# Optimization experiments

Hardware: AMD Instinct MI355X
Metric: run time of the kernel (lower is better)

The kernel has to match this reference:

```python
import jax, jax.numpy as jnp
import numpy as np

N_NODES = 100000

def _glorot(key, shape):
    lim = np.sqrt(6.0 / (shape[0] + shape[1])).astype(np.float32)
    return jax.random.uniform(key, shape, jnp.float32, -lim, lim)

def setup_inputs() -> dict:
    key = jax.random.key(0)
    ks = jax.random.split(key, 9)
    x = jax.random.normal(ks[0], (N_NODES, 256), jnp.float32)
    edge_index = jax.random.randint(ks[1], (2, 1600000), 0, N_NODES, jnp.int32)
    dims = [(256, 256), (256, 256), (256, 40)]
    params = {}
    for i, (din, dout) in enumerate(dims):
        params[f"Wl{i}"] = _glorot(ks[2 + 2 * i], (din, dout))   # neighbor (lin_l) weight
        params[f"Wr{i}"] = _glorot(ks[3 + 2 * i], (din, dout))   # root (lin_r) weight
        params[f"b{i}"] = jnp.zeros((dout,), jnp.float32)
    return {"x": x, "edge_index": edge_index, **params}

def _sage_conv(x, src, dst, Wl, Wr, b):
    # mean-aggregate neighbor features at destination nodes, then linear
    msg_sum = jax.ops.segment_sum(x[src], dst, num_segments=N_NODES)      # [N, d]
    deg = jax.ops.segment_sum(jnp.ones((src.shape[0],), x.dtype), dst,
                              num_segments=N_NODES)                       # [N]
    mean = msg_sum / jnp.maximum(deg, 1.0)[:, None]
    return mean @ Wl + x @ Wr + b

def reference(x, edge_index, Wl0, Wr0, b0, Wl1, Wr1, b1, Wl2, Wr2, b2):
    src, dst = edge_index[0], edge_index[1]
    h = jax.nn.relu(_sage_conv(x, src, dst, Wl0, Wr0, b0))
    h = jax.nn.relu(_sage_conv(h, src, dst, Wl1, Wr1, b1))
    h = _sage_conv(h, src, dst, Wl2, Wr2, b2)
    return jax.nn.log_softmax(h, axis=1)
```

## Files before the change

kernel.cpp:

```cpp
#include <hip/hip_runtime.h>
#include <hip/hip_bf16.h>
#include <math.h>

#define N_NODES 100000
#define N_EDGES 1600000
#define DIN 256
#define KTOT 512
#define SLOTS 64

typedef __attribute__((ext_vector_type(8))) short frag_ab;
typedef __attribute__((ext_vector_type(4))) float frag_cd;

__device__ inline unsigned short f2bf(float f) {
    union { float f; unsigned u; } v; v.f = f;
    unsigned r = v.u + 0x7FFF + ((v.u >> 16) & 1);
    return (unsigned short)(r >> 16);
}
__device__ inline float bf2f(unsigned u16) {
    union { unsigned u; float f; } v; v.u = u16 << 16;
    return v.f;
}
__device__ inline float bf_lo(unsigned u) {
    union { unsigned u; float f; } v; v.u = u << 16; return v.f;
}
__device__ inline float bf_hi(unsigned u) {
    union { unsigned u; float f; } v; v.u = u & 0xffff0000u; return v.f;
}

__global__ void build_bucket(const int* __restrict__ src, const int* __restrict__ dst,
                             int* __restrict__ cnt, int* __restrict__ col, int nE) {
    int e = blockIdx.x * blockDim.x + threadIdx.x;
    if (e >= nE) return;
    int d = dst[e];
    int pos = atomicAdd(&cnt[d], 1);
    if (pos < SLOTS) col[(size_t)d * SLOTS + pos] = src[e];
}

__global__ void conv_f32_bf16(const float* __restrict__ x, unsigned short* __restrict__ y, int n4) {
    int i = blockIdx.x * blockDim.x + threadIdx.x;
    if (i >= n4) return;
    float4 v = ((const float4*)x)[i];
    uint2 o;
    o.x = (unsigned)f2bf(v.x) | ((unsigned)f2bf(v.y) << 16);
    o.y = (unsigned)f2bf(v.z) | ((unsigned)f2bf(v.w) << 16);
    ((uint2*)y)[i] = o;
}

__global__ void conv_weights(const float* __restrict__ Wl0, const float* __restrict__ Wr0,
                             const float* __restrict__ Wl1, const float* __restrict__ Wr1,
                             const float* __restrict__ Wl2, const float* __restrict__ Wr2,
                             unsigned short* __restrict__ Wt0, unsigned short* __restrict__ Wt1,
                             unsigned short* __restrict__ Wl2t, unsigned short* __restrict__ Wr2t) {
    int idx = blockIdx.x * blockDim.x + threadIdx.x;
    if (idx < 262144) {
        const float* Wl = (idx < 131072) ? Wl0 : Wl1;
        const float* Wr = (idx < 131072) ? Wr0 : Wr1;
        unsigned short* Wt = (idx < 131072) ? Wt0 : Wt1;
        int i = idx & 131071;
        int n = i >> 9, k = i & 511;
        float v = (k < 256) ? Wl[k * 256 + n] : Wr[(k - 256) * 256 + n];
        Wt[i] = f2bf(v);
    } else if (idx < 294912) {
        const float* W = (idx < 278528) ? Wl2 : Wr2;
        unsigned short* Wt = (idx < 278528) ? Wl2t : Wr2t;
        int i = (idx - 262144) & 16383;
        int n = i >> 8, k = i & 255;
        Wt[i] = f2bf((n < 40) ? W[k * 40 + n] : 0.f);
    }
}

__global__ __launch_bounds__(256) void gather_mean_bf(
    const int* __restrict__ cnt, const int* __restrict__ col,
    const unsigned short* __restrict__ h, unsigned short* __restrict__ mean, int nNodes) {
    int node = blockIdx.x * 4 + (threadIdx.x >> 6);
    int lane = threadIdx.x & 63;
    if (node >= nNodes) return;
    int deg = cnt[node];
    int nd = (deg < SLOTS) ? deg : SLOTS;
    const int* cp = col + (size_t)node * SLOTS;
    int half = lane >> 5;
    int l = lane & 31;
    float a0 = 0, a1 = 0, a2 = 0, a3 = 0, a4 = 0, a5 = 0, a6 = 0, a7 = 0;
    int e = 0;
    for (; e + 8 <= nd; e += 8) {
        int s0 = cp[e + half];
        int s1 = cp[e + 2 + half];
        int s2 = cp[e + 4 + half];
        int s3 = cp[e + 6 + half];
        uint4 v0 = *(const uint4*)(h + (size_t)s0 * DIN + l * 8);
        uint4 v1 = *(const uint4*)(h + (size_t)s1 * DIN + l * 8);
        uint4 v2 = *(const uint4*)(h + (size_t)s2 * DIN + l * 8);
        uint4 v3 = *(const uint4*)(h + (size_t)s3 * DIN + l * 8);
        a0 += bf_lo(v0.x); a1 += bf_hi(v0.x); a2 += bf_lo(v0.y); a3 += bf_hi(v0.y);
        a4 += bf_lo(v0.z); a5 += bf_hi(v0.z); a6 += bf_lo(v0.w); a7 += bf_hi(v0.w);
        a0 += bf_lo(v1.x); a1 += bf_hi(v1.x); a2 += bf_lo(v1.y); a3 += bf_hi(v1.y);
        a4 += bf_lo(v1.z); a5 += bf_hi(v1.z); a6 += bf_lo(v1.w); a7 += bf_hi(v1.w);
        a0 += bf_lo(v2.x); a1 += bf_hi(v2.x); a2 += bf_lo(v2.y); a3 += bf_hi(v2.y);
        a4 += bf_lo(v2.z); a5 += bf_hi(v2.z); a6 += bf_lo(v2.w); a7 += bf_hi(v2.w);
        a0 += bf_lo(v3.x); a1 += bf_hi(v3.x); a2 += bf_lo(v3.y); a3 += bf_hi(v3.y);
        a4 += bf_lo(v3.z); a5 += bf_hi(v3.z); a6 += bf_lo(v3.w); a7 += bf_hi(v3.w);
    }
    for (; e + 2 <= nd; e += 2) {
        int s = cp[e + half];
        uint4 v = *(const uint4*)(h + (size_t)s * DIN + l * 8);
        a0 += bf_lo(v.x); a1 += bf_hi(v.x); a2 += bf_lo(v.y); a3 += bf_hi(v.y);
        a4 += bf_lo(v.z); a5 += bf_hi(v.z); a6 += bf_lo(v.w); a7 += bf_hi(v.w);
    }
    if (e < nd && half == 0) {
        int s = cp[e];
        uint4 v = *(const uint4*)(h + (size_t)s * DIN + l * 8);
        a0 += bf_lo(v.x); a1 += bf_hi(v.x); a2 += bf_lo(v.y); a3 += bf_hi(v.y);
        a4 += bf_lo(v.z); a5 += bf_hi(v.z); a6 += bf_lo(v.w); a7 += bf_hi(v.w);
    }
    a0 += __shfl_xor(a0, 32); a1 += __shfl_xor(a1, 32);
    a2 += __shfl_xor(a2, 32); a3 += __shfl_xor(a3, 32);
    a4 += __shfl_xor(a4, 32); a5 += __shfl_xor(a5, 32);
    a6 += __shfl_xor(a6, 32); a7 += __shfl_xor(a7, 32);
    if (half == 0) {
        float inv = 1.0f / fmaxf((float)deg, 1.0f);
        uint4 o;
        o.x = (unsigned)f2bf(a0 * inv) | ((unsigned)f2bf(a1 * inv) << 16);
        o.y = (unsigned)f2bf(a2 * inv) | ((unsigned)f2bf(a3 * inv) << 16);
        o.z = (unsigned)f2bf(a4 * inv) | ((unsigned)f2bf(a5 * inv) << 16);
        o.w = (unsigned)f2bf(a6 * inv) | ((unsigned)f2bf(a7 * inv) << 16);
        *(uint4*)(mean + (size_t)node * DIN + l * 8) = o;
    }
}

__global__ __launch_bounds__(256) void gather_mean64(
    const int* __restrict__ cnt, const int* __restrict__ col,
    const unsigned short* __restrict__ z, unsigned short* __restrict__ mz, int nNodes) {
    int node = blockIdx.x * 4 + (threadIdx.x >> 6);
    int lane = threadIdx.x & 63;
    if (node >= nNodes) return;
    int deg = cnt[node];
    int nd = (deg < SLOTS) ? deg : SLOTS;
    const int* cp = col + (size_t)node * SLOTS;
    int g = lane >> 4;
    int l = lane & 15;
    float a0 = 0, a1 = 0, a2 = 0, a3 = 0;
    int e = 0;
    for (; e + 8 <= nd; e += 8) {
        int s0 = cp[e + g];
        int s1 = cp[e + 4 + g];
        uint2 v0 = *(const uint2*)(z + (size_t)s0 * 64 + l * 4);
        uint2 v1 = *(const uint2*)(z + (size_t)s1 * 64 + l * 4);
        a0 += bf_lo(v0.x); a1 += bf_hi(v0.x); a2 += bf_lo(v0.y); a3 += bf_hi(v0.y);
        a0 += bf_lo(v1.x); a1 += bf_hi(v1.x); a2 += bf_lo(v1.y); a3 += bf_hi(v1.y);
    }
    for (; e + 4 <= nd; e += 4) {
        int s = cp[e + g];
        uint2 v = *(const uint2*)(z + (size_t)s * 64 + l * 4);
        a0 += bf_lo(v.x); a1 += bf_hi(v.x); a2 += bf_lo(v.y); a3 += bf_hi(v.y);
    }
    int rem = nd - e;
    if (g < rem) {
        int s = cp[e + g];
        uint2 v = *(const uint2*)(z + (size_t)s * 64 + l * 4);
        a0 += bf_lo(v.x); a1 += bf_hi(v.x); a2 += bf_lo(v.y); a3 += bf_hi(v.y);
    }
    a0 += __shfl_xor(a0, 16); a1 += __shfl_xor(a1, 16);
    a2 += __shfl_xor(a2, 16); a3 += __shfl_xor(a3, 16);
    a0 += __shfl_xor(a0, 32); a1 += __shfl_xor(a1, 32);
    a2 += __shfl_xor(a2, 32); a3 += __shfl_xor(a3, 32);
    if (lane < 16) {
        float inv = 1.0f / fmaxf((float)deg, 1.0f);
        uint2 o;
        o.x = (unsigned)f2bf(a0 * inv) | ((unsigned)f2bf(a1 * inv) << 16);
        o.y = (unsigned)f2bf(a2 * inv) | ((unsigned)f2bf(a3 * inv) << 16);
        *(uint2*)(mz + (size_t)node * 64 + l * 4) = o;
    }
}

template <bool RELU>
__global__ __launch_bounds__(256) void sage_mfma(
    const unsigned short* __restrict__ mean, const unsigned short* __restrict__ h,
    const unsigned short* __restrict__ Wt, const float* __restrict__ bias,
    unsigned short* __restrict__ out, int nNodes) {
    __shared__ unsigned short sA[64][32];
    __shared__ unsigned short sB[256][32];

    int tid = threadIdx.x;
    int wave = tid >> 6;
    int lane = tid & 63;
    int lrow = lane & 15;
    int quad = lane >> 4;
    int node0 = blockIdx.x * 64;

    frag_cd acc[4][4];
#pragma unroll
    for (int mi = 0; mi < 4; mi++)
#pragma unroll
        for (int ni = 0; ni < 4; ni++) acc[mi][ni] = (frag_cd){0.f, 0.f, 0.f, 0.f};

    int ar = tid >> 2;
    int ak = (tid & 3) * 8;
    int aNode = node0 + ar;

    for (int kb = 0; kb < KTOT; kb += 32) {
        {
            const unsigned short* srcp = (kb < 256)
                ? (mean + (size_t)aNode * DIN + kb + ak)
                : (h + (size_t)aNode * DIN + (kb - 256) + ak);
            uint4 av = {0u, 0u, 0u, 0u};
            if (aNode < nNodes) av = *(const uint4*)srcp;
            *(uint4*)(&sA[ar][ak]) = av;
        }
        {
            const unsigned short* wp = Wt + (size_t)tid * KTOT + kb;
#pragma unroll
            for (int j = 0; j < 4; j++)
                *(uint4*)(&sB[tid][j * 8]) = *(const uint4*)(wp + j * 8);
        }
        __syncthreads();

        frag_ab aF[4], bF[4];
#pragma unroll
        for (int mi = 0; mi < 4; mi++)
            aF[mi] = *(const frag_ab*)(&sA[mi * 16 + lrow][quad * 8]);
#pragma unroll
        for (int ni = 0; ni < 4; ni++)
            bF[ni] = *(const frag_ab*)(&sB[(wave * 4 + ni) * 16 + lrow][quad * 8]);

#pragma unroll
        for (int mi = 0; mi < 4; mi++)
#pragma unroll
            for (int ni = 0; ni < 4; ni++)
                acc[mi][ni] = __builtin_amdgcn_mfma_f32_16x16x32_bf16(
                    aF[mi], bF[ni], acc[mi][ni], 0, 0, 0);
        __syncthreads();
    }

#pragma unroll
    for (int ni = 0; ni < 4; ni++) {
        int colc = (wave * 4 + ni) * 16 + lrow;
        float bv = bias[colc];
#pragma unroll
        for (int mi = 0; mi < 4; mi++) {
#pragma unroll
            for (int r = 0; r < 4; r++) {
                int node = node0 + mi * 16 + quad * 4 + r;
                if (node < nNodes) {
                    float v = acc[mi][ni][r] + bv;
                    if (RELU) v = fmaxf(v, 0.f);
                    out[(size_t)node * 256 + colc] = f2bf(v);
                }
            }
        }
    }
}

__global__ __launch_bounds__(256) void mfma_lin64(
    const unsigned short* __restrict__ h, const unsigned short* __restrict__ Wt,
    unsigned short* __restrict__ z, int nNodes) {
    __shared__ unsigned short sA[64][32];
    __shared__ unsigned short sB[64][32];

    int tid = threadIdx.x;
    int wave = tid >> 6;
    int lane = tid & 63;
    int lrow = lane & 15;
    int quad = lane >> 4;
    int node0 = blockIdx.x * 64;

    frag_cd acc[4];
#pragma unroll
    for (int ni = 0; ni < 4; ni++) acc[ni] = (frag_cd){0.f, 0.f, 0.f, 0.f};

    int ar = tid >> 2;
    int ak = (tid & 3) * 8;
    int aNode = node0 + ar;

    for (int kb = 0; kb < 256; kb += 32) {
        uint4 av = {0u, 0u, 0u, 0u};
        if (aNode < nNodes) av = *(const uint4*)(h + (size_t)aNode * DIN + kb + ak);
        *(uint4*)(&sA[ar][ak]) = av;
        *(uint4*)(&sB[ar][ak]) = *(const uint4*)(Wt + (size_t)ar * 256 + kb + ak);
        __syncthreads();

        frag_ab aF = *(const frag_ab*)(&sA[wave * 16 + lrow][quad * 8]);
#pragma unroll
        for (int ni = 0; ni < 4; ni++) {
            frag_ab bF = *(const frag_ab*)(&sB[ni * 16 + lrow][quad * 8]);
            acc[ni] = __builtin_amdgcn_mfma_f32_16x16x32_bf16(aF, bF, acc[ni], 0, 0, 0);
        }
        __syncthreads();
    }

#pragma unroll
    for (int ni = 0; ni < 4; ni++) {
        int colc = ni * 16 + lrow;
#pragma unroll
        for (int r = 0; r < 4; r++) {
            int node = node0 + wave * 16 + quad * 4 + r;
            if (node < nNodes)
                z[(size_t)node * 64 + colc] = f2bf(acc[ni][r]);
        }
    }
}

__global__ __launch_bounds__(256) void sage_out(
    const unsigned short* __restrict__ h, const unsigned short* __restrict__ Wt,
    const unsigned short* __restrict__ mz, const float* __restrict__ bias,
    float* __restrict__ out, int nNodes) {
    __shared__ unsigned short sA[64][32];
    __shared__ unsigned short sB[64][32];

    int tid = threadIdx.x;
    int wave = tid >> 6;
    int lane = tid & 63;
    int lrow = lane & 15;
    int quad = lane >> 4;
    int node0 = blockIdx.x * 64;

    frag_cd acc[4];
#pragma unroll
    for (int ni = 0; ni < 4; ni++) acc[ni] = (frag_cd){0.f, 0.f, 0.f, 0.f};

    int ar = tid >> 2;
    int ak = (tid & 3) * 8;
    int aNode = node0 + ar;

    for (int kb = 0; kb < 256; kb += 32) {
        uint4 av = {0u, 0u, 0u, 0u};
        if (aNode < nNodes) av = *(const uint4*)(h + (size_t)aNode * DIN + kb + ak);
        *(uint4*)(&sA[ar][ak]) = av;
        *(uint4*)(&sB[ar][ak]) = *(const uint4*)(Wt + (size_t)ar * 256 + kb + ak);
        __syncthreads();

        frag_ab aF = *(const frag_ab*)(&sA[wave * 16 + lrow][quad * 8]);
#pragma unroll
        for (int ni = 0; ni < 4; ni++) {
            frag_ab bF = *(const frag_ab*)(&sB[ni * 16 + lrow][quad * 8]);
            acc[ni] = __builtin_amdgcn_mfma_f32_16x16x32_bf16(aF, bF, acc[ni], 0, 0, 0);
        }
        __syncthreads();
    }

#pragma unroll
    for (int r = 0; r < 4; r++) {
        int node = node0 + wave * 16 + quad * 4 + r;
        bool valid = (node < nNodes);
        float v[4];
#pragma unroll
        for (int ni = 0; ni < 4; ni++) {
            int colc = ni * 16 + lrow;
            if (colc < 40 && valid)
                v[ni] = acc[ni][r] + bias[colc] + bf2f(mz[(size_t)node * 64 + colc]);
            else
                v[ni] = -INFINITY;
        }
        float m = fmaxf(fmaxf(v[0], v[1]), fmaxf(v[2], v[3]));
#pragma unroll
        for (int off = 1; off < 16; off <<= 1) m = fmaxf(m, __shfl_xor(m, off));
        float s = 0.f;
#pragma unroll
        for (int ni = 0; ni < 4; ni++)
            if (v[ni] != -INFINITY) s += expf(v[ni] - m);
#pragma unroll
        for (int off = 1; off < 16; off <<= 1) s += __shfl_xor(s, off);
        float ls = logf(s);
#pragma unroll
        for (int ni = 0; ni < 4; ni++) {
            int colc = ni * 16 + lrow;
            if (valid && colc < 40)
                out[(size_t)node * 40 + colc] = v[ni] - m - ls;
        }
    }
}

extern "C" void kernel_launch(void* const* d_in, const int* in_sizes, int n_in,
                              void* d_out, int out_size, void* d_ws, size_t ws_size,
                              hipStream_t stream) {
    const float* x   = (const float*)d_in[0];
    const int*   ei  = (const int*)d_in[1];
    const float* Wl0 = (const float*)d_in[2];
    const float* Wr0 = (const float*)d_in[3];
    const float* b0  = (const float*)d_in[4];
    const float* Wl1 = (const float*)d_in[5];
    const float* Wr1 = (const float*)d_in[6];
    const float* b1  = (const float*)d_in[7];
    const float* Wl2 = (const float*)d_in[8];
    const float* Wr2 = (const float*)d_in[9];
    const float* b2  = (const float*)d_in[10];
    float* out = (float*)d_out;

    const int* src = ei;
    const int* dst = ei + N_EDGES;

    const size_t NODE_PAD = 100352;
    char* ws = (char*)d_ws;
    int* cnt  = (int*)ws;  ws += NODE_PAD * sizeof(int);
    int* colv = (int*)ws;  ws += (size_t)NODE_PAD * SLOTS * sizeof(int);
    unsigned short* xbf  = (unsigned short*)ws; ws += (size_t)N_NODES * DIN * sizeof(unsigned short);
    unsigned short* mean = (unsigned short*)ws; ws += (size_t)N_NODES * DIN * sizeof(unsigned short);
    unsigned short* h1   = (unsigned short*)ws; ws += (size_t)N_NODES * DIN * sizeof(unsigned short);
    unsigned short* h2   = (unsigned short*)ws; ws += (size_t)N_NODES * DIN * sizeof(unsigned short);
    unsigned short* zb   = (unsigned short*)ws; ws += (size_t)N_NODES * 64 * sizeof(unsigned short);
    unsigned short* mz   = (unsigned short*)ws; ws += (size_t)N_NODES * 64 * sizeof(unsigned short);
    unsigned short* Wt0  = (unsigned short*)ws; ws += 256 * KTOT * sizeof(unsigned short);
    unsigned short* Wt1  = (unsigned short*)ws; ws += 256 * KTOT * sizeof(unsigned short);
    unsigned short* Wl2t = (unsigned short*)ws; ws += 64 * 256 * sizeof(unsigned short);
    unsigned short* Wr2t = (unsigned short*)ws; ws += 64 * 256 * sizeof(unsigned short);

    hipMemsetAsync(cnt, 0, N_NODES * sizeof(int), stream);
    build_bucket<<<(N_EDGES + 255) / 256, 256, 0, stream>>>(src, dst, cnt, colv, N_EDGES);

    conv_f32_bf16<<<(N_NODES * DIN / 4 + 255) / 256, 256, 0, stream>>>(x, xbf, N_NODES * DIN / 4);
    conv_weights<<<(294912 + 255) / 256, 256, 0, stream>>>(Wl0, Wr0, Wl1, Wr1, Wl2, Wr2,
                                                           Wt0, Wt1, Wl2t, Wr2t);

    const int gatherBlocks = (N_NODES + 3) / 4;
    const int mfmaBlocks = (N_NODES + 63) / 64;

    gather_mean_bf<<<gatherBlocks, 256, 0, stream>>>(cnt, colv, xbf, mean, N_NODES);
    sage_mfma<true><<<mfmaBlocks, 256, 0, stream>>>(mean, xbf, Wt0, b0, h1, N_NODES);

    gather_mean_bf<<<gatherBlocks, 256, 0, stream>>>(cnt, colv, h1, mean, N_NODES);
    sage_mfma<true><<<mfmaBlocks, 256, 0, stream>>>(mean, h1, Wt1, b1, h2, N_NODES);

    mfma_lin64<<<mfmaBlocks, 256, 0, stream>>>(h2, Wl2t, zb, N_NODES);
    gather_mean64<<<gatherBlocks, 256, 0, stream>>>(cnt, colv, zb, mz, N_NODES);
    sage_out<<<mfmaBlocks, 256, 0, stream>>>(h2, Wr2t, mz, b2, out, N_NODES);
}
```

Measured before the change: 777.4 us.

## Fuse prep kernels into one launch and fold layer-3 projection into layer-2 GEMM

Merges edge bucketing, weight conversion and x conversion into one prep kernel with block-range dispatch. It also fuses the layer-2 SAGE GEMM with the layer-3 neighbor projection (h2 @ Wl2). The h2 tile is staged in LDS, each wave handles a 64-wide K slice, and partial products are reduced through LDS atomics before zb is written. This removes a re-read of h2 from global memory and a launch. In exchange it uses about 50KB of LDS per block, which may lower occupancy, and adds shared-memory atomics.

```diff
diff --git a/kernel.cpp b/kernel.cpp
--- a/kernel.cpp
+++ b/kernel.cpp
@@ -27,45 +27,46 @@
     union { unsigned u; float f; } v; v.u = u & 0xffff0000u; return v.f;
 }
 
-__global__ void build_bucket(const int* __restrict__ src, const int* __restrict__ dst,
-                             int* __restrict__ cnt, int* __restrict__ col, int nE) {
-    int e = blockIdx.x * blockDim.x + threadIdx.x;
-    if (e >= nE) return;
-    int d = dst[e];
-    int pos = atomicAdd(&cnt[d], 1);
-    if (pos < SLOTS) col[(size_t)d * SLOTS + pos] = src[e];
-}
-
-__global__ void conv_f32_bf16(const float* __restrict__ x, unsigned short* __restrict__ y, int n4) {
-    int i = blockIdx.x * blockDim.x + threadIdx.x;
-    if (i >= n4) return;
-    float4 v = ((const float4*)x)[i];
-    uint2 o;
-    o.x = (unsigned)f2bf(v.x) | ((unsigned)f2bf(v.y) << 16);
-    o.y = (unsigned)f2bf(v.z) | ((unsigned)f2bf(v.w) << 16);
-    ((uint2*)y)[i] = o;
-}
-
-__global__ void conv_weights(const float* __restrict__ Wl0, const float* __restrict__ Wr0,
-                             const float* __restrict__ Wl1, const float* __restrict__ Wr1,
-                             const float* __restrict__ Wl2, const float* __restrict__ Wr2,
-                             unsigned short* __restrict__ Wt0, unsigned short* __restrict__ Wt1,
-                             unsigned short* __restrict__ Wl2t, unsigned short* __restrict__ Wr2t) {
-    int idx = blockIdx.x * blockDim.x + threadIdx.x;
-    if (idx < 262144) {
-        const float* Wl = (idx < 131072) ? Wl0 : Wl1;
-        const float* Wr = (idx < 131072) ? Wr0 : Wr1;
-        unsigned short* Wt = (idx < 131072) ? Wt0 : Wt1;
-        int i = idx & 131071;
-        int n = i >> 9, k = i & 511;
-        float v = (k < 256) ? Wl[k * 256 + n] : Wr[(k - 256) * 256 + n];
-        Wt[i] = f2bf(v);
-    } else if (idx < 294912) {
-        const float* W = (idx < 278528) ? Wl2 : Wr2;
-        unsigned short* Wt = (idx < 278528) ? Wl2t : Wr2t;
-        int i = (idx - 262144) & 16383;
-        int n = i >> 8, k = i & 255;
-        Wt[i] = f2bf((n < 40) ? W[k * 40 + n] : 0.f);
+__global__ __launch_bounds__(256) void prep(
+    const int* __restrict__ src, const int* __restrict__ dst,
+    int* __restrict__ cnt, int* __restrict__ col,
+    const float* __restrict__ x, unsigned short* __restrict__ xbf,
+    const float* __restrict__ Wl0, const float* __restrict__ Wr0,
+    const float* __restrict__ Wl1, const float* __restrict__ Wr1,
+    const float* __restrict__ Wl2, const float* __restrict__ Wr2,
+    unsigned short* __restrict__ Wt0, unsigned short* __restrict__ Wt1,
+    unsigned short* __restrict__ Wl2t, unsigned short* __restrict__ Wr2t) {
+    int b = blockIdx.x;
+    int tid = threadIdx.x;
+    if (b < 6250) {
+        int e = b * 256 + tid;
+        int d = dst[e];
+        int pos = atomicAdd(&cnt[d], 1);
+        if (pos < SLOTS) col[(size_t)d * SLOTS + pos] = src[e];
+    } else if (b < 7402) {
+        int idx = (b - 6250) * 256 + tid;
+        if (idx < 262144) {
+            const float* Wl = (idx < 131072) ? Wl0 : Wl1;
+            const float* Wr = (idx < 131072) ? Wr0 : Wr1;
+            unsigned short* Wt = (idx < 131072) ? Wt0 : Wt1;
+            int i = idx & 131071;
+            int n = i >> 9, k = i & 511;
+            float v = (k < 256) ? Wl[k * 256 + n] : Wr[(k - 256) * 256 + n];
+            Wt[i] = f2bf(v);
+        } else if (idx < 294912) {
+            const float* W = (idx < 278528) ? Wl2 : Wr2;
+            unsigned short* Wt = (idx < 278528) ? Wl2t : Wr2t;
+            int i = (idx - 262144) & 16383;
+            int n = i >> 8, k = i & 255;
+            Wt[i] = f2bf((n < 40) ? W[k * 40 + n] : 0.f);
+        }
+    } else {
+        int i = (b - 7402) * 256 + tid;
+        float4 v = ((const float4*)x)[i];
+        uint2 o;
+        o.x = (unsigned)f2bf(v.x) | ((unsigned)f2bf(v.y) << 16);
+        o.y = (unsigned)f2bf(v.z) | ((unsigned)f2bf(v.w) << 16);
+        ((uint2*)xbf)[i] = o;
     }
 }
 
@@ -172,7 +173,6 @@
     }
 }
 
-template <bool RELU>
 __global__ __launch_bounds__(256) void sage_mfma(
     const unsigned short* __restrict__ mean, const unsigned short* __restrict__ h,
     const unsigned short* __restrict__ Wt, const float* __restrict__ bias,
@@ -241,8 +241,7 @@
             for (int r = 0; r < 4; r++) {
                 int node = node0 + mi * 16 + quad * 4 + r;
                 if (node < nNodes) {
-                    float v = acc[mi][ni][r] + bv;
-                    if (RELU) v = fmaxf(v, 0.f);
+                    float v = fmaxf(acc[mi][ni][r] + bv, 0.f);
                     out[(size_t)node * 256 + colc] = f2bf(v);
                 }
             }
@@ -250,11 +249,17 @@
     }
 }
 
-__global__ __launch_bounds__(256) void mfma_lin64(
-    const unsigned short* __restrict__ h, const unsigned short* __restrict__ Wt,
-    unsigned short* __restrict__ z, int nNodes) {
-    __shared__ unsigned short sA[64][32];
-    __shared__ unsigned short sB[64][32];
+#define H2P 264
+__global__ __launch_bounds__(256) void sage_mfma1z(
+    const unsigned short* __restrict__ mean, const unsigned short* __restrict__ h,
+    const unsigned short* __restrict__ Wt, const float* __restrict__ bias,
+    const unsigned short* __restrict__ Wl2t,
+    unsigned short* __restrict__ out, unsigned short* __restrict__ zb, int nNodes) {
+    __shared__ __align__(16) char smem[50176];
+    unsigned short* sA = (unsigned short*)smem;
+    unsigned short* sB = (unsigned short*)(smem + 4096);
+    unsigned short* h2t = (unsigned short*)smem;
+    float* zacc = (float*)(smem + 33792);
 
     int tid = threadIdx.x;
     int wave = tid >> 6;
@@ -263,38 +268,118 @@
     int quad = lane >> 4;
     int node0 = blockIdx.x * 64;
 
-    frag_cd acc[4];
-#pragma unroll
-    for (int ni = 0; ni < 4; ni++) acc[ni] = (frag_cd){0.f, 0.f, 0.f, 0.f};
+    frag_cd acc[4][4];
+#pragma unroll
+    for (int mi = 0; mi < 4; mi++)
+#pragma unroll
+        for (int ni = 0; ni < 4; ni++) acc[mi][ni] = (frag_cd){0.f, 0.f, 0.f, 0.f};
 
     int ar = tid >> 2;
     int ak = (tid & 3) * 8;
     int aNode = node0 + ar;
 
-    for (int kb = 0; kb < 256; kb += 32) {
-        uint4 av = {0u, 0u, 0u, 0u};
-        if (aNode < nNodes) av = *(const uint4*)(h + (size_t)aNode * DIN + kb + ak);
-        *(uint4*)(&sA[ar][ak]) = av;
-        *(uint4*)(&sB[ar][ak]) = *(const uint4*)(Wt + (size_t)ar * 256 + kb + ak);
+    for (int kb = 0; kb < KTOT; kb += 32) {
+        {
+            const unsigned short* srcp = (kb < 256)
+                ? (mean + (size_t)aNode * DIN + kb + ak)
+                : (h + (size_t)aNode * DIN + (kb - 256) + ak);
+            uint4 av = {0u, 0u, 0u, 0u};
+            if (aNode < nNodes) av = *(const uint4*)srcp;
+            *(uint4*)(sA + ar * 32 + ak) = av;
+        }
+        {
+            const unsigned short* wp = Wt + (size_t)tid * KTOT + kb;
+#pragma unroll
+            for (int j = 0; j < 4; j++)
+                *(uint4*)(sB + tid * 32 + j * 8) = *(const uint4*)(wp + j * 8);
+        }
         __syncthreads();
 
-        frag_ab aF = *(const frag_ab*)(&sA[wave * 16 + lrow][quad * 8]);
-#pragma unroll
-        for (int ni = 0; ni < 4; ni++) {
-            frag_ab bF = *(const frag_ab*)(&sB[ni * 16 + lrow][quad * 8]);
-            acc[ni] = __builtin_amdgcn_mfma_f32_16x16x32_bf16(aF, bF, acc[ni], 0, 0, 0);
-        }
+        frag_ab aF[4], bF[4];
+#pragma unroll
+        for (int mi = 0; mi < 4; mi++)
+            aF[mi] = *(const frag_ab*)(sA + (mi * 16 + lrow) * 32 + quad * 8);
+#pragma unroll
+        for (int ni = 0; ni < 4; ni++)
+            bF[ni] = *(const frag_ab*)(sB + ((wave * 4 + ni) * 16 + lrow) * 32 + quad * 8);
+
+#pragma unroll
+        for (int mi = 0; mi < 4; mi++)
+#pragma unroll
+            for (int ni = 0; ni < 4; ni++)
+                acc[mi][ni] = __builtin_amdgcn_mfma_f32_16x16x32_bf16(
+                    aF[mi], bF[ni], acc[mi][ni], 0, 0, 0);
         __syncthreads();
     }
 
 #pragma unroll
     for (int ni = 0; ni < 4; ni++) {
-        int colc = ni * 16 + lrow;
-#pragma unroll
-        for (int r = 0; r < 4; r++) {
-            int node = node0 + wave * 16 + quad * 4 + r;
-            if (node < nNodes)
-                z[(size_t)node * 64 + colc] = f2bf(acc[ni][r]);
+        int colc = (wave * 4 + ni) * 16 + lrow;
+        float bv = bias[colc];
+#pragma unroll
+        for (int mi = 0; mi < 4; mi++) {
+#pragma unroll
+            for (int r = 0; r < 4; r++) {
+                int row = mi * 16 + quad * 4 + r;
+                int node = node0 + row;
+                float v = fmaxf(acc[mi][ni][r] + bv, 0.f);
+                unsigned short bv16 = f2bf(v);
+                h2t[row * H2P + colc] = bv16;
+                if (node < nNodes) out[(size_t)node * 256 + colc] = bv16;
+            }
+        }
+    }
+#pragma unroll
+    for (int j = 0; j < 16; j++) zacc[tid + j * 256] = 0.f;
+    __syncthreads();
+
+    frag_cd acc2[4][4];
+#pragma unroll
+    for (int mi = 0; mi < 4; mi++)
+#pragma unroll
+        for (int ni = 0; ni < 4; ni++) acc2[mi][ni] = (frag_cd){0.f, 0.f, 0.f, 0.f};
+
+#pragma unroll
+    for (int kk = 0; kk < 64; kk += 32) {
+        int kbase = wave * 64 + kk;
+        frag_ab aF[4], bF[4];
+#pragma unroll
+        for (int mi = 0; mi < 4; mi++)
+            aF[mi] = *(const frag_ab*)(h2t + (mi * 16 + lrow) * H2P + kbase + quad * 8);
+#pragma unroll
+        for (int ni = 0; ni < 4; ni++)
+            bF[ni] = *(const frag_ab*)(Wl2t + (size_t)(ni * 16 + lrow) * 256 + kbase + quad * 8);
+#pragma unroll
+        for (int mi = 0; mi < 4; mi++)
+#pragma unroll
+            for (int ni = 0; ni < 4; ni++)
+                acc2[mi][ni] = __builtin_amdgcn_mfma_f32_16x16x32_bf16(
+                    aF[mi], bF[ni], acc2[mi][ni], 0, 0, 0);
+    }
+#pragma unroll
+    for (int mi = 0; mi < 4; mi++)
+#pragma unroll
+        for (int ni = 0; ni < 4; ni++)
+#pragma unroll
+            for (int r = 0; r < 4; r++)
+                atomicAdd(&zacc[(mi * 16 + quad * 4 + r) * 64 + ni * 16 + lrow],
+                          acc2[mi][ni][r]);
+    __syncthreads();
+
+    {
+        int nn = tid >> 2;
+        int c0 = (tid & 3) * 16;
+        int node = node0 + nn;
+        if (node < nNodes) {
+            const float* zp = zacc + nn * 64 + c0;
+            unsigned w[8];
+#pragma unroll
+            for (int j = 0; j < 8; j++)
+                w[j] = (unsigned)f2bf(zp[2 * j]) | ((unsigned)f2bf(zp[2 * j + 1]) << 16);
+            uint4 o0 = {w[0], w[1], w[2], w[3]};
+            uint4 o1 = {w[4], w[5], w[6], w[7]};
+            *(uint4*)(zb + (size_t)node * 64 + c0) = o0;
+            *(uint4*)(zb + (size_t)node * 64 + c0 + 8) = o1;
         }
     }
 }
@@ -404,22 +489,19 @@
     unsigned short* Wr2t = (unsigned short*)ws; ws += 64 * 256 * sizeof(unsigned short);
 
     hipMemsetAsync(cnt, 0, N_NODES * sizeof(int), stream);
-    build_bucket<<<(N_EDGES + 255) / 256, 256, 0, stream>>>(src, dst, cnt, colv, N_EDGES);
-
-    conv_f32_bf16<<<(N_NODES * DIN / 4 + 255) / 256, 256, 0, stream>>>(x, xbf, N_NODES * DIN / 4);
-    conv_weights<<<(294912 + 255) / 256, 256, 0, stream>>>(Wl0, Wr0, Wl1, Wr1, Wl2, Wr2,
-                                                           Wt0, Wt1, Wl2t, Wr2t);
+    prep<<<32402, 256, 0, stream>>>(src, dst, cnt, colv, x, xbf,
+                                    Wl0, Wr0, Wl1, Wr1, Wl2, Wr2,
+                                    Wt0, Wt1, Wl2t, Wr2t);
 
     const int gatherBlocks = (N_NODES + 3) / 4;
     const int mfmaBlocks = (N_NODES + 63) / 64;
 
     gather_mean_bf<<<gatherBlocks, 256, 0, stream>>>(cnt, colv, xbf, mean, N_NODES);
-    sage_mfma<true><<<mfmaBlocks, 256, 0, stream>>>(mean, xbf, Wt0, b0, h1, N_NODES);
+    sage_mfma<<<mfmaBlocks, 256, 0, stream>>>(mean, xbf, Wt0, b0, h1, N_NODES);
 
     gather_mean_bf<<<gatherBlocks, 256, 0, stream>>>(cnt, colv, h1, mean, N_NODES);
-    sage_mfma<true><<<mfmaBlocks, 256, 0, stream>>>(mean, h1, Wt1, b1, h2, N_NODES);
-
-    mfma_lin64<<<mfmaBlocks, 256, 0, stream>>>(h2, Wl2t, zb, N_NODES);
+    sage_mfma1z<<<mfmaBlocks, 256, 0, stream>>>(mean, h1, Wt1, b1, Wl2t, h2, zb, N_NODES);
+
     gather_mean64<<<gatherBlocks, 256, 0, stream>>>(cnt, colv, zb, mz, N_NODES);
     sage_out<<<mfmaBlocks, 256, 0, stream>>>(h2, Wr2t, mz, b2, out, N_NODES);
 }
```

Result: slower. 891.9 us (+14.7%).

## Tile neighbor gather by feature column slices and fuse prep kernels

Applied to the files above, without the earlier changes.

Replaces the full-row gather (one wave per node reading 512B rows) with a 2D grid where each block handles a 32-byte column slice (16 features) for a node. The intent is to keep the gathered feature slice resident in cache across neighbors, since all nodes touching the same tile hit a 3.2MB working set rather than the full 51MB table. The cost is that column indices are re-read once per tile and each load is only 4 bytes per lane. Separately, the edge bucketing, weight conversion and x conversion kernels are merged into one launch to save launch overhead.

```diff
diff --git a/kernel.cpp b/kernel.cpp
--- a/kernel.cpp
+++ b/kernel.cpp
@@ -27,152 +27,95 @@
     union { unsigned u; float f; } v; v.u = u & 0xffff0000u; return v.f;
 }
 
-__global__ void build_bucket(const int* __restrict__ src, const int* __restrict__ dst,
-                             int* __restrict__ cnt, int* __restrict__ col, int nE) {
-    int e = blockIdx.x * blockDim.x + threadIdx.x;
-    if (e >= nE) return;
-    int d = dst[e];
-    int pos = atomicAdd(&cnt[d], 1);
-    if (pos < SLOTS) col[(size_t)d * SLOTS + pos] = src[e];
-}
-
-__global__ void conv_f32_bf16(const float* __restrict__ x, unsigned short* __restrict__ y, int n4) {
-    int i = blockIdx.x * blockDim.x + threadIdx.x;
-    if (i >= n4) return;
-    float4 v = ((const float4*)x)[i];
-    uint2 o;
-    o.x = (unsigned)f2bf(v.x) | ((unsigned)f2bf(v.y) << 16);
-    o.y = (unsigned)f2bf(v.z) | ((unsigned)f2bf(v.w) << 16);
-    ((uint2*)y)[i] = o;
-}
-
-__global__ void conv_weights(const float* __restrict__ Wl0, const float* __restrict__ Wr0,
-                             const float* __restrict__ Wl1, const float* __restrict__ Wr1,
-                             const float* __restrict__ Wl2, const float* __restrict__ Wr2,
-                             unsigned short* __restrict__ Wt0, unsigned short* __restrict__ Wt1,
-                             unsigned short* __restrict__ Wl2t, unsigned short* __restrict__ Wr2t) {
-    int idx = blockIdx.x * blockDim.x + threadIdx.x;
-    if (idx < 262144) {
-        const float* Wl = (idx < 131072) ? Wl0 : Wl1;
-        const float* Wr = (idx < 131072) ? Wr0 : Wr1;
-        unsigned short* Wt = (idx < 131072) ? Wt0 : Wt1;
-        int i = idx & 131071;
-        int n = i >> 9, k = i & 511;
-        float v = (k < 256) ? Wl[k * 256 + n] : Wr[(k - 256) * 256 + n];
-        Wt[i] = f2bf(v);
-    } else if (idx < 294912) {
-        const float* W = (idx < 278528) ? Wl2 : Wr2;
-        unsigned short* Wt = (idx < 278528) ? Wl2t : Wr2t;
-        int i = (idx - 262144) & 16383;
-        int n = i >> 8, k = i & 255;
-        Wt[i] = f2bf((n < 40) ? W[k * 40 + n] : 0.f);
-    }
-}
-
-__global__ __launch_bounds__(256) void gather_mean_bf(
+__global__ __launch_bounds__(256) void prep(
+    const int* __restrict__ src, const int* __restrict__ dst,
+    int* __restrict__ cnt, int* __restrict__ col,
+    const float* __restrict__ x, unsigned short* __restrict__ xbf,
+    const float* __restrict__ Wl0, const float* __restrict__ Wr0,
+    const float* __restrict__ Wl1, const float* __restrict__ Wr1,
+    const float* __restrict__ Wl2, const float* __restrict__ Wr2,
+    unsigned short* __restrict__ Wt0, unsigned short* __restrict__ Wt1,
+    unsigned short* __restrict__ Wl2t, unsigned short* __restrict__ Wr2t) {
+    int b = blockIdx.x;
+    int tid = threadIdx.x;
+    if (b < 6250) {
+        int e = b * 256 + tid;
+        int d = dst[e];
+        int pos = atomicAdd(&cnt[d], 1);
+        if (pos < SLOTS) col[(size_t)d * SLOTS + pos] = src[e];
+    } else if (b < 7402) {
+        int idx = (b - 6250) * 256 + tid;
+        if (idx < 262144) {
+            const float* Wl = (idx < 131072) ? Wl0 : Wl1;
+            const float* Wr = (idx < 131072) ? Wr0 : Wr1;
+            unsigned short* Wt = (idx < 131072) ? Wt0 : Wt1;
+            int i = idx & 131071;
+            int n = i >> 9, k = i & 511;
+            float v = (k < 256) ? Wl[k * 256 + n] : Wr[(k - 256) * 256 + n];
+            Wt[i] = f2bf(v);
+        } else if (idx < 294912) {
+            const float* W = (idx < 278528) ? Wl2 : Wr2;
+            unsigned short* Wt = (idx < 278528) ? Wl2t : Wr2t;
+            int i = (idx - 262144) & 16383;
+            int n = i >> 8, k = i & 255;
+            Wt[i] = f2bf((n < 40) ? W[k * 40 + n] : 0.f);
+        }
+    } else {
+        int i = (b - 7402) * 256 + tid;
+        float4 v = ((const float4*)x)[i];
+        uint2 o;
+        o.x = (unsigned)f2bf(v.x) | ((unsigned)f2bf(v.y) << 16);
+        o.y = (unsigned)f2bf(v.z) | ((unsigned)f2bf(v.w) << 16);
+        ((uint2*)xbf)[i] = o;
+    }
+}
+
+template <int W>
+__global__ __launch_bounds__(256) void gather_tile(
     const int* __restrict__ cnt, const int* __restrict__ col,
     const unsigned short* __restrict__ h, unsigned short* __restrict__ mean, int nNodes) {
     int node = blockIdx.x * 4 + (threadIdx.x >> 6);
+    int tile = blockIdx.y;
     int lane = threadIdx.x & 63;
     if (node >= nNodes) return;
     int deg = cnt[node];
     int nd = (deg < SLOTS) ? deg : SLOTS;
     const int* cp = col + (size_t)node * SLOTS;
-    int half = lane >> 5;
-    int l = lane & 31;
-    float a0 = 0, a1 = 0, a2 = 0, a3 = 0, a4 = 0, a5 = 0, a6 = 0, a7 = 0;
+    int g = lane >> 3;
+    int sl = lane & 7;
+    const unsigned short* hb = h + tile * 16 + sl * 2;
+    float a0 = 0.f, a1 = 0.f;
     int e = 0;
-    for (; e + 8 <= nd; e += 8) {
-        int s0 = cp[e + half];
-        int s1 = cp[e + 2 + half];
-        int s2 = cp[e + 4 + half];
-        int s3 = cp[e + 6 + half];
-        uint4 v0 = *(const uint4*)(h + (size_t)s0 * DIN + l * 8);
-        uint4 v1 = *(const uint4*)(h + (size_t)s1 * DIN + l * 8);
-        uint4 v2 = *(const uint4*)(h + (size_t)s2 * DIN + l * 8);
-        uint4 v3 = *(const uint4*)(h + (size_t)s3 * DIN + l * 8);
-        a0 += bf_lo(v0.x); a1 += bf_hi(v0.x); a2 += bf_lo(v0.y); a3 += bf_hi(v0.y);
-        a4 += bf_lo(v0.z); a5 += bf_hi(v0.z); a6 += bf_lo(v0.w); a7 += bf_hi(v0.w);
-        a0 += bf_lo(v1.x); a1 += bf_hi(v1.x); a2 += bf_lo(v1.y); a3 += bf_hi(v1.y);
-        a4 += bf_lo(v1.z); a5 += bf_hi(v1.z); a6 += bf_lo(v1.w); a7 += bf_hi(v1.w);
-        a0 += bf_lo(v2.x); a1 += bf_hi(v2.x); a2 += bf_lo(v2.y); a3 += bf_hi(v2.y);
-        a4 += bf_lo(v2.z); a5 += bf_hi(v2.z); a6 += bf_lo(v2.w); a7 += bf_hi(v2.w);
-        a0 += bf_lo(v3.x); a1 += bf_hi(v3.x); a2 += bf_lo(v3.y); a3 += bf_hi(v3.y);
-        a4 += bf_lo(v3.z); a5 += bf_hi(v3.z); a6 += bf_lo(v3.w); a7 += bf_hi(v3.w);
-    }
-    for (; e + 2 <= nd; e += 2) {
-        int s = cp[e + half];
-        uint4 v = *(const uint4*)(h + (size_t)s * DIN + l * 8);
-        a0 += bf_lo(v.x); a1 += bf_hi(v.x); a2 += bf_lo(v.y); a3 += bf_hi(v.y);
-        a4 += bf_lo(v.z); a5 += bf_hi(v.z); a6 += bf_lo(v.w); a7 += bf_hi(v.w);
-    }
-    if (e < nd && half == 0) {
-        int s = cp[e];
-        uint4 v = *(const uint4*)(h + (size_t)s * DIN + l * 8);
-        a0 += bf_lo(v.x); a1 += bf_hi(v.x); a2 += bf_lo(v.y); a3 += bf_hi(v.y);
-        a4 += bf_lo(v.z); a5 += bf_hi(v.z); a6 += bf_lo(v.w); a7 += bf_hi(v.w);
-    }
-    a0 += __shfl_xor(a0, 32); a1 += __shfl_xor(a1, 32);
-    a2 += __shfl_xor(a2, 32); a3 += __shfl_xor(a3, 32);
-    a4 += __shfl_xor(a4, 32); a5 += __shfl_xor(a5, 32);
-    a6 += __shfl_xor(a6, 32); a7 += __shfl_xor(a7, 32);
-    if (half == 0) {
-        float inv = 1.0f / fmaxf((float)deg, 1.0f);
-        uint4 o;
-        o.x = (unsigned)f2bf(a0 * inv) | ((unsigned)f2bf(a1 * inv) << 16);
-        o.y = (unsigned)f2bf(a2 * inv) | ((unsigned)f2bf(a3 * inv) << 16);
-        o.z = (unsigned)f2bf(a4 * inv) | ((unsigned)f2bf(a5 * inv) << 16);
-        o.w = (unsigned)f2bf(a6 * inv) | ((unsigned)f2bf(a7 * inv) << 16);
-        *(uint4*)(mean + (size_t)node * DIN + l * 8) = o;
-    }
-}
-
-__global__ __launch_bounds__(256) void gather_mean64(
-    const int* __restrict__ cnt, const int* __restrict__ col,
-    const unsigned short* __restrict__ z, unsigned short* __restrict__ mz, int nNodes) {
-    int node = blockIdx.x * 4 + (threadIdx.x >> 6);
-    int lane = threadIdx.x & 63;
-    if (node >= nNodes) return;
-    int deg = cnt[node];
-    int nd = (deg < SLOTS) ? deg : SLOTS;
-    const int* cp = col + (size_t)node * SLOTS;
-    int g = lane >> 4;
-    int l = lane & 15;
-    float a0 = 0, a1 = 0, a2 = 0, a3 = 0;
-    int e = 0;
-    for (; e + 8 <= nd; e += 8) {
+    for (; e + 16 <= nd; e += 16) {
         int s0 = cp[e + g];
-        int s1 = cp[e + 4 + g];
-        uint2 v0 = *(const uint2*)(z + (size_t)s0 * 64 + l * 4);
-        uint2 v1 = *(const uint2*)(z + (size_t)s1 * 64 + l * 4);
-        a0 += bf_lo(v0.x); a1 += bf_hi(v0.x); a2 += bf_lo(v0.y); a3 += bf_hi(v0.y);
-        a0 += bf_lo(v1.x); a1 += bf_hi(v1.x); a2 += bf_lo(v1.y); a3 += bf_hi(v1.y);
-    }
-    for (; e + 4 <= nd; e += 4) {
+        int s1 = cp[e + 8 + g];
+        unsigned v0 = *(const unsigned*)(hb + (size_t)s0 * W);
+        unsigned v1 = *(const unsigned*)(hb + (size_t)s1 * W);
+        a0 += bf_lo(v0) + bf_lo(v1);
+        a1 += bf_hi(v0) + bf_hi(v1);
+    }
+    if (e + 8 <= nd) {
         int s = cp[e + g];
-        uint2 v = *(const uint2*)(z + (size_t)s * 64 + l * 4);
-        a0 += bf_lo(v.x); a1 += bf_hi(v.x); a2 += bf_lo(v.y); a3 += bf_hi(v.y);
+        unsigned v = *(const unsigned*)(hb + (size_t)s * W);
+        a0 += bf_lo(v); a1 += bf_hi(v);
+        e += 8;
     }
     int rem = nd - e;
     if (g < rem) {
         int s = cp[e + g];
-        uint2 v = *(const uint2*)(z + (size_t)s * 64 + l * 4);
-        a0 += bf_lo(v.x); a1 += bf_hi(v.x); a2 += bf_lo(v.y); a3 += bf_hi(v.y);
-    }
+        unsigned v = *(const unsigned*)(hb + (size_t)s * W);
+        a0 += bf_lo(v); a1 += bf_hi(v);
+    }
+    a0 += __shfl_xor(a0, 8);  a1 += __shfl_xor(a1, 8);
     a0 += __shfl_xor(a0, 16); a1 += __shfl_xor(a1, 16);
-    a2 += __shfl_xor(a2, 16); a3 += __shfl_xor(a3, 16);
     a0 += __shfl_xor(a0, 32); a1 += __shfl_xor(a1, 32);
-    a2 += __shfl_xor(a2, 32); a3 += __shfl_xor(a3, 32);
-    if (lane < 16) {
+    if (g == 0) {
         float inv = 1.0f / fmaxf((float)deg, 1.0f);
-        uint2 o;
-        o.x = (unsigned)f2bf(a0 * inv) | ((unsigned)f2bf(a1 * inv) << 16);
-        o.y = (unsigned)f2bf(a2 * inv) | ((unsigned)f2bf(a3 * inv) << 16);
-        *(uint2*)(mz + (size_t)node * 64 + l * 4) = o;
-    }
-}
-
-template <bool RELU>
+        unsigned o = (unsigned)f2bf(a0 * inv) | ((unsigned)f2bf(a1 * inv) << 16);
+        *(unsigned*)(mean + (size_t)node * W + tile * 16 + sl * 2) = o;
+    }
+}
+
 __global__ __launch_bounds__(256) void sage_mfma(
     const unsigned short* __restrict__ mean, const unsigned short* __restrict__ h,
     const unsigned short* __restrict__ Wt, const float* __restrict__ bias,
@@ -241,8 +184,7 @@
             for (int r = 0; r < 4; r++) {
                 int node = node0 + mi * 16 + quad * 4 + r;
                 if (node < nNodes) {
-                    float v = acc[mi][ni][r] + bv;
-                    if (RELU) v = fmaxf(v, 0.f);
+                    float v = fmaxf(acc[mi][ni][r] + bv, 0.f);
                     out[(size_t)node * 256 + colc] = f2bf(v);
                 }
             }
@@ -404,22 +346,20 @@
     unsigned short* Wr2t = (unsigned short*)ws; ws += 64 * 256 * sizeof(unsigned short);
 
     hipMemsetAsync(cnt, 0, N_NODES * sizeof(int), stream);
-    build_bucket<<<(N_EDGES + 255) / 256, 256, 0, stream>>>(src, dst, cnt, colv, N_EDGES);
-
-    conv_f32_bf16<<<(N_NODES * DIN / 4 + 255) / 256, 256, 0, stream>>>(x, xbf, N_NODES * DIN / 4);
-    conv_weights<<<(294912 + 255) / 256, 256, 0, stream>>>(Wl0, Wr0, Wl1, Wr1, Wl2, Wr2,
-                                                           Wt0, Wt1, Wl2t, Wr2t);
-
-    const int gatherBlocks = (N_NODES + 3) / 4;
+    prep<<<32402, 256, 0, stream>>>(src, dst, cnt, colv, x, xbf,
+                                    Wl0, Wr0, Wl1, Wr1, Wl2, Wr2,
+                                    Wt0, Wt1, Wl2t, Wr2t);
+
+    const int nodeBlocks = (N_NODES + 3) / 4;
     const int mfmaBlocks = (N_NODES + 63) / 64;
 
-    gather_mean_bf<<<gatherBlocks, 256, 0, stream>>>(cnt, colv, xbf, mean, N_NODES);
-    sage_mfma<true><<<mfmaBlocks, 256, 0, stream>>>(mean, xbf, Wt0, b0, h1, N_NODES);
-
-    gather_mean_bf<<<gatherBlocks, 256, 0, stream>>>(cnt, colv, h1, mean, N_NODES);
-    sage_mfma<true><<<mfmaBlocks, 256, 0, stream>>>(mean, h1, Wt1, b1, h2, N_NODES);
+    gather_tile<256><<<dim3(nodeBlocks, 16), 256, 0, stream>>>(cnt, colv, xbf, mean, N_NODES);
+    sage_mfma<<<mfmaBlocks, 256, 0, stream>>>(mean, xbf, Wt0, b0, h1, N_NODES);
+
+    gather_tile<256><<<dim3(nodeBlocks, 16), 256, 0, stream>>>(cnt, colv, h1, mean, N_NODES);
+    sage_mfma<<<mfmaBlocks, 256, 0, stream>>>(mean, h1, Wt1, b1, h2, N_NODES);
 
     mfma_lin64<<<mfmaBlocks, 256, 0, stream>>>(h2, Wl2t, zb, N_NODES);
-    gather_mean64<<<gatherBlocks, 256, 0, stream>>>(cnt, colv, zb, mz, N_NODES);
+    gather_tile<64><<<dim3(nodeBlocks, 4), 256, 0, stream>>>(cnt, colv, zb, mz, N_NODES);
     sage_out<<<mfmaBlocks, 256, 0, stream>>>(h2, Wr2t, mz, b2, out, N_NODES);
 }
```

Measured after the change: 1.588 ms. 2.04x slower.
